# Optimization experiments

Hardware: AMD Instinct MI355X
Metric: run time of the kernel (lower is better)

## Reference

```python
import jax, jax.numpy as jnp
import numpy as np

# Model dims (from ModelArgs defaults)
B, S, DIM = 1, 1024, 2880
H, HKV, HD = 64, 8, 64        # query heads, kv heads, head dim
GROUP = H // HKV              # 8 query heads per kv head
WINDOW = 128                  # sliding window (layer_idx=0 -> active)
THETA = 150000.0


def setup_inputs() -> dict:
    key = jax.random.key(0)
    ks = jax.random.split(key, 10)
    rn = lambda k, shape, sc: (jax.random.normal(k, shape, jnp.float32) * sc)
    return {
        "x": rn(ks[0], (B, S, DIM), 1.0),
        "wq_w": rn(ks[1], (H * HD, DIM), 0.02),
        "wq_b": rn(ks[2], (H * HD,), 0.02),
        "wk_w": rn(ks[3], (HKV * HD, DIM), 0.02),
        "wk_b": rn(ks[4], (HKV * HD,), 0.02),
        "wv_w": rn(ks[5], (HKV * HD, DIM), 0.02),
        "wv_b": rn(ks[6], (HKV * HD,), 0.02),
        "wo_w": rn(ks[7], (DIM, H * HD), 0.02),
        "wo_b": rn(ks[8], (DIM,), 0.02),
        "sinks": rn(ks[9], (H,), 1.0),
    }


def _rope(t):
    # t: [B, S, h, HD]; half-split (rotate_half) RoPE with base THETA
    half = HD // 2
    inv_freq = 1.0 / (THETA ** (jnp.arange(half, dtype=jnp.float32) * 2.0 / HD))
    ang = jnp.arange(S, dtype=jnp.float32)[:, None] * inv_freq      # [S, half]
    cos = jnp.cos(ang)[None, :, None, :]
    sin = jnp.sin(ang)[None, :, None, :]
    t1, t2 = t[..., :half], t[..., half:]
    return jnp.concatenate([t1 * cos - t2 * sin, t1 * sin + t2 * cos], axis=-1)


def reference(x, wq_w, wq_b, wk_w, wk_b, wv_w, wv_b, wo_w, wo_b, sinks):
    # Projections (nn.Linear: y = x @ W^T + b)
    q = (jnp.einsum('bsd,ed->bse', x, wq_w) + wq_b).reshape(B, S, H, HD)
    k = (jnp.einsum('bsd,ed->bse', x, wk_w) + wk_b).reshape(B, S, HKV, HD)
    v = (jnp.einsum('bsd,ed->bse', x, wv_w) + wv_b).reshape(B, S, HKV, HD)

    q = _rope(q)
    k = _rope(k)

    # GQA: expand kv heads to match query heads
    k = jnp.repeat(k, GROUP, axis=2)   # [B, S, H, HD]
    v = jnp.repeat(v, GROUP, axis=2)

    scale = HD ** -0.5
    scores = jnp.einsum('bihd,bjhd->bhij', q, k) * scale   # [B, H, S, S]

    # Causal + sliding-window mask: attend to j with 0 <= i-j < WINDOW
    i = jnp.arange(S)[:, None]
    j = jnp.arange(S)[None, :]
    allowed = (j <= i) & ((i - j) < WINDOW)
    scores = jnp.where(allowed, scores, jnp.float32(-1e30))

    # Softmax with per-head learnable sink logit folded into normalization
    sink = sinks[None, :, None, None]                       # [1, H, 1, 1]
    m = jnp.maximum(jnp.max(scores, axis=-1, keepdims=True), sink)
    e = jnp.exp(scores - m)
    denom = jnp.sum(e, axis=-1, keepdims=True) + jnp.exp(sink - m)
    probs = e / denom                                       # sink mass dropped

    out = jnp.einsum('bhij,bjhd->bihd', probs, v).reshape(B, S, H * HD)
    return jnp.einsum('bse,de->bsd', out, wo_w) + wo_b
```

## Files before the change

### kernel.cpp

```cpp
#include <hip/hip_runtime.h>

typedef __attribute__((ext_vector_type(4))) float f32x4;
typedef __attribute__((ext_vector_type(8))) short s16x8;
typedef unsigned short u16;

#define DEVI __device__ __forceinline__

DEVI u16 f2bf(float f) {
    union { float f; unsigned int u; } v; v.f = f;
    unsigned int r = v.u + 0x7FFFu + ((v.u >> 16) & 1u);
    return (u16)(r >> 16);
}
DEVI float bf2f(u16 b) {
    union { unsigned int u; float f; } v; v.u = ((unsigned int)b) << 16;
    return v.f;
}

typedef __attribute__((address_space(1))) void gv_t;
typedef __attribute__((address_space(3))) void sv_t;

#define GLOAD16(SRC, DST) __builtin_amdgcn_global_load_lds( \
    (gv_t*)(SRC), (sv_t*)(DST), 16, 0, 0)

DEVI f32x4 mfma_bf16(s16x8 a, s16x8 b, f32x4 c) {
    return __builtin_amdgcn_mfma_f32_16x16x32_bf16(a, b, c, 0, 0, 0);
}

__global__ void cvt1_kernel(
    const float* __restrict__ x,  const float* __restrict__ wq, const float* __restrict__ wk,
    const float* __restrict__ wv,
    u16* __restrict__ xb, u16* __restrict__ wqb, u16* __restrict__ wkb,
    u16* __restrict__ wvb)
{
    int id = blockIdx.x * 256 + threadIdx.x;
    const float* s; u16* d; int off;
    if      (id < 737280)  { s = x;  d = xb;  off = id; }
    else if (id < 3686400) { s = wq; d = wqb; off = id - 737280; }
    else if (id < 4055040) { s = wk; d = wkb; off = id - 3686400; }
    else                   { s = wv; d = wvb; off = id - 4055040; }
    f32x4 v = *(const f32x4*)(s + (size_t)off * 4);
    union { u16 u[4]; unsigned long long ll; } o;
    #pragma unroll
    for (int j = 0; j < 4; ++j) o.u[j] = f2bf(v[j]);
    *(unsigned long long*)(d + (size_t)off * 4) = o.ll;
}

__global__ void cvt_wo_kernel(const float* __restrict__ wo, u16* __restrict__ wob)
{
    int id = blockIdx.x * 256 + threadIdx.x;
    f32x4 v = *(const f32x4*)(wo + (size_t)id * 4);
    union { u16 u[4]; unsigned long long ll; } o;
    #pragma unroll
    for (int j = 0; j < 4; ++j) o.u[j] = f2bf(v[j]);
    *(unsigned long long*)(wob + (size_t)id * 4) = o.ll;
}

__global__ __launch_bounds__(256, 2) void gemm_bf16nt(
    const u16* __restrict__ A, int lda, int kit, int ntot,
    const u16* __restrict__ W0, int t0, int n0, int c0,
    const u16* __restrict__ W1, int t1, int n1, int c1,
    const u16* __restrict__ W2, int t2, int n2, int c2,
    u16* __restrict__ C, int ldc, long long cstride)
{
    __shared__ u16 Als[2][128 * 64];
    __shared__ u16 Bls[2][128 * 64];

    const int lin = blockIdx.x;
    const int xc  = lin & 7;
    const int mm  = lin >> 3;
    const int nbl = xc + 8 * (mm >> 3);
    const int yt  = mm & 7;
    if (nbl >= ntot) return;

    const int tid  = threadIdx.x;
    const int lane = tid & 63;
    const int wid  = tid >> 6;
    const int li   = lane & 15;
    const int lg   = lane >> 4;
    const int m0   = yt * 128;

    const u16* W; int nt0, nsz, cb;
    if (nbl < t0)           { W = W0; nt0 = nbl * 128;             nsz = n0; cb = c0; }
    else if (nbl < t0 + t1) { W = W1; nt0 = (nbl - t0) * 128;      nsz = n1; cb = c1; }
    else                    { W = W2; nt0 = (nbl - t0 - t1) * 128; nsz = n2; cb = c2; }

    const int z  = blockIdx.z;
    const int S  = gridDim.z;
    const int it0 = (z * kit) / S;
    const int it1 = ((z + 1) * kit) / S;
    u16* Cp = C + (long long)z * cstride;

    const int wm = (wid >> 1) * 64;
    const int wn = (wid & 1) * 64;

    f32x4 acc[4][4];
    #pragma unroll
    for (int mi = 0; mi < 4; ++mi)
        #pragma unroll
        for (int ni = 0; ni < 4; ++ni)
            acc[mi][ni] = (f32x4){0.f, 0.f, 0.f, 0.f};

    const int srow = tid >> 3;
    const int slc  = (tid & 7) ^ (srow & 7);

#define STAGE(BUF, IT)                                                          \
    do {                                                                        \
        int k0_ = (IT) * 64;                                                    \
        _Pragma("unroll")                                                       \
        for (int s_ = 0; s_ < 4; ++s_) {                                        \
            const u16* sa_ = A + (size_t)(m0 + s_ * 32 + srow) * lda + k0_ + slc * 8; \
            GLOAD16(sa_, &Als[BUF][(s_ * 256 + wid * 64) * 8]);                 \
        }                                                                       \
        _Pragma("unroll")                                                       \
        for (int s_ = 0; s_ < 4; ++s_) {                                        \
            int wr_ = nt0 + s_ * 32 + srow;                                     \
            if (wr_ > nsz - 1) wr_ = nsz - 1;                                   \
            const u16* sb_ = W + (size_t)wr_ * lda + k0_ + slc * 8;             \
            GLOAD16(sb_, &Bls[BUF][(s_ * 256 + wid * 64) * 8]);                 \
        }                                                                       \
    } while (0)

    STAGE(0, it0);
    asm volatile("" ::: "memory");
    STAGE(1, it0 + 1);

    for (int it = it0; it < it1; ++it) {
        const int cur = (it - it0) & 1;

        if (it + 1 < it1) {
            asm volatile("s_waitcnt vmcnt(8)\n\ts_barrier" ::: "memory");
        } else {
            asm volatile("s_waitcnt vmcnt(0)\n\ts_barrier" ::: "memory");
        }

        s16x8 af[4][2], bfv[4][2];
        #pragma unroll
        for (int mi = 0; mi < 4; ++mi)
            #pragma unroll
            for (int kc = 0; kc < 2; ++kc) {
                int row = wm + mi * 16 + li;
                int ch  = (kc * 4 + lg) ^ (row & 7);
                af[mi][kc] = *(const s16x8*)&Als[cur][row * 64 + ch * 8];
            }
        #pragma unroll
        for (int ni = 0; ni < 4; ++ni)
            #pragma unroll
            for (int kc = 0; kc < 2; ++kc) {
                int row = wn + ni * 16 + li;
                int ch  = (kc * 4 + lg) ^ (row & 7);
                bfv[ni][kc] = *(const s16x8*)&Bls[cur][row * 64 + ch * 8];
            }
        #pragma unroll
        for (int mi = 0; mi < 4; ++mi)
            #pragma unroll
            for (int ni = 0; ni < 4; ++ni)
                #pragma unroll
                for (int kc = 0; kc < 2; ++kc)
                    acc[mi][ni] = mfma_bf16(af[mi][kc], bfv[ni][kc], acc[mi][ni]);

        asm volatile("s_waitcnt lgkmcnt(0)\n\ts_barrier" ::: "memory");

        if (it + 2 < it1) STAGE(cur, it + 2);
    }
#undef STAGE

    #pragma unroll
    for (int ni = 0; ni < 4; ++ni) {
        int colr = nt0 + wn + ni * 16 + li;
        if (colr < nsz) {
            #pragma unroll
            for (int mi = 0; mi < 4; ++mi)
                #pragma unroll
                for (int r = 0; r < 4; ++r) {
                    int row = m0 + wm + mi * 16 + lg * 4 + r;
                    Cp[(size_t)row * ldc + cb + colr] = f2bf(acc[mi][ni][r]);
                }
        }
    }
}

__global__ void rope_kernel(const u16* __restrict__ qkvp,
                            const float* __restrict__ qb, const float* __restrict__ kb,
                            const float* __restrict__ vb,
                            u16* __restrict__ qo, u16* __restrict__ ko, u16* __restrict__ vo)
{
    const long long PST = 1024LL * 5120;
    int id = blockIdx.x * 256 + threadIdx.x;
    int s  = id / 2560;
    int r  = id % 2560;
    const u16* r0 = qkvp + (size_t)s * 5120;
    if (r < 2304) {
        bool isq = r < 2048;
        int rr   = isq ? r : r - 2048;
        int hh   = rr >> 5;
        int d    = rr & 31;
        int col  = (isq ? 0 : 4096) + hh * 64 + d;
        int bcol = isq ? col : col - 4096;
        const float* bias = isq ? qb : kb;
        float t1 = bf2f(r0[col])      + bf2f(r0[col + PST])      + bf2f(r0[col + 2 * PST])      + bias[bcol];
        float t2 = bf2f(r0[col + 32]) + bf2f(r0[col + 32 + PST]) + bf2f(r0[col + 32 + 2 * PST]) + bias[bcol + 32];
        float ang = (float)s * exp2f((float)d * -0.5373314f);
        float sn, cs;
        sincosf(ang, &sn, &cs);
        float sc = isq ? 0.125f : 1.0f;
        float o1 = (t1 * cs - t2 * sn) * sc;
        float o2 = (t1 * sn + t2 * cs) * sc;
        u16* dst = isq ? qo : ko;
        int ldd  = isq ? 4096 : 512;
        dst[(size_t)s * ldd + bcol]      = f2bf(o1);
        dst[(size_t)s * ldd + bcol + 32] = f2bf(o2);
    } else {
        int e = (r - 2304) * 2;
        int c0 = 4608 + e;
        float v0 = bf2f(r0[c0])     + bf2f(r0[c0 + PST])     + bf2f(r0[c0 + 2 * PST])     + vb[e];
        float v1 = bf2f(r0[c0 + 1]) + bf2f(r0[c0 + 1 + PST]) + bf2f(r0[c0 + 1 + 2 * PST]) + vb[e + 1];
        vo[(size_t)s * 512 + e]     = f2bf(v0);
        vo[(size_t)s * 512 + e + 1] = f2bf(v1);
    }
}

__global__ void reduce_out_kernel(const u16* __restrict__ parts,
                                  const float* __restrict__ bias,
                                  float* __restrict__ out)
{
    int id = blockIdx.x * 256 + threadIdx.x;
    const long long stride = 1024LL * 2880;
    long long base = (long long)id * 8;
    float s[8];
    #pragma unroll
    for (int j = 0; j < 8; ++j) s[j] = 0.f;
    #pragma unroll
    for (int p = 0; p < 5; ++p) {
        s16x8 v = *(const s16x8*)(parts + p * stride + base);
        #pragma unroll
        for (int j = 0; j < 8; ++j) s[j] += bf2f((u16)v[j]);
    }
    int cb = (int)(base % 2880);
    f32x4 b0 = *(const f32x4*)(bias + cb);
    f32x4 b1 = *(const f32x4*)(bias + cb + 4);
    f32x4 o0 = {s[0] + b0[0], s[1] + b0[1], s[2] + b0[2], s[3] + b0[3]};
    f32x4 o1 = {s[4] + b1[0], s[5] + b1[1], s[6] + b1[2], s[7] + b1[3]};
    *(f32x4*)(out + base)     = o0;
    *(f32x4*)(out + base + 4) = o1;
}

__global__ __launch_bounds__(256, 2) void attn_kernel(
    const u16* __restrict__ Q, const u16* __restrict__ Kb, const u16* __restrict__ Vb,
    const float* __restrict__ sinks, u16* __restrict__ Ob)
{
    __shared__ u16 Kls[64 * 64];
    __shared__ u16 Pls[4][16 * 72];

    const int h    = blockIdx.x;
    const int qblk = blockIdx.y;
    const int kvh  = h >> 3;
    const int tid  = threadIdx.x;
    const int lane = tid & 63;
    const int w    = tid >> 6;
    const int li   = lane & 15;
    const int lg   = lane >> 4;
    const int qw   = qblk * 64 + w * 16;

    s16x8 aq[2];
    {
        const u16* qrow = Q + ((size_t)(qw + li) * 64 + h) * 64 + lg * 8;
        aq[0] = *(const s16x8*)(qrow);
        aq[1] = *(const s16x8*)(qrow + 32);
    }

    const float snk = sinks[h];
    float m_run[4], l_run[4];
    f32x4 oacc[4];
    #pragma unroll
    for (int r = 0; r < 4; ++r) { m_run[r] = snk; l_run[r] = 1.0f; }
    #pragma unroll
    for (int ni = 0; ni < 4; ++ni) oacc[ni] = (f32x4){0.f, 0.f, 0.f, 0.f};

    const int srow = tid >> 3;
    const int slc  = (tid & 7) ^ (srow & 7);

    for (int t = 0; t < 3; ++t) {
        int jt = qblk - 2 + t;
        if (jt < 0) continue;
        int j0 = jt * 64;

        #pragma unroll
        for (int it = 0; it < 2; ++it) {
            const u16* src = Kb + ((size_t)(j0 + it * 32 + srow) * 8 + kvh) * 64 + slc * 8;
            GLOAD16(src, &Kls[(it * 256 + w * 64) * 8]);
        }
        __syncthreads();

        f32x4 sc[4];
        #pragma unroll
        for (int nf = 0; nf < 4; ++nf) {
            sc[nf] = (f32x4){0.f, 0.f, 0.f, 0.f};
            #pragma unroll
            for (int kc = 0; kc < 2; ++kc) {
                int row = nf * 16 + li;
                int ch  = (kc * 4 + lg) ^ (row & 7);
                s16x8 bk = *(const s16x8*)&Kls[row * 64 + ch * 8];
                sc[nf] = mfma_bf16(aq[kc], bk, sc[nf]);
            }
        }

        #pragma unroll
        for (int r = 0; r < 4; ++r) {
            const int qg = qw + lg * 4 + r;
            float mx = -1e30f;
            #pragma unroll
            for (int nf = 0; nf < 4; ++nf) {
                int jg = j0 + nf * 16 + li;
                bool ok = (jg <= qg) && (qg - jg < 128);
                float v = ok ? sc[nf][r] : -1e30f;
                sc[nf][r] = v;
                mx = fmaxf(mx, v);
            }
            #pragma unroll
            for (int off = 1; off < 16; off <<= 1)
                mx = fmaxf(mx, __shfl_xor(mx, off));
            float mnew = fmaxf(m_run[r], mx);
            float corr = __expf(m_run[r] - mnew);
            m_run[r] = mnew;
            float rs = 0.f;
            #pragma unroll
            for (int nf = 0; nf < 4; ++nf) {
                float p = __expf(sc[nf][r] - mnew);
                rs += p;
                Pls[w][(lg * 4 + r) * 72 + nf * 16 + li] = f2bf(p);
            }
            #pragma unroll
            for (int off = 1; off < 16; off <<= 1)
                rs += __shfl_xor(rs, off);
            l_run[r] = l_run[r] * corr + rs;
            #pragma unroll
            for (int ni = 0; ni < 4; ++ni) oacc[ni][r] *= corr;
        }
        __syncthreads();

        #pragma unroll
        for (int kc = 0; kc < 2; ++kc) {
            s16x8 pa = *(const s16x8*)&Pls[w][li * 72 + kc * 32 + lg * 8];
            #pragma unroll
            for (int ni = 0; ni < 4; ++ni) {
                const u16* vsrc = Vb + ((size_t)(j0 + kc * 32 + lg * 8) * 8 + kvh) * 64 + ni * 16 + li;
                s16x8 bv;
                #pragma unroll
                for (int i = 0; i < 8; ++i) bv[i] = (short)vsrc[(size_t)i * 512];
                oacc[ni] = mfma_bf16(pa, bv, oacc[ni]);
            }
        }
    }

    #pragma unroll
    for (int r = 0; r < 4; ++r) {
        float inv = 1.0f / l_run[r];
        #pragma unroll
        for (int ni = 0; ni < 4; ++ni)
            Ob[((size_t)(qw + lg * 4 + r) * 64 + h) * 64 + ni * 16 + li] = f2bf(oacc[ni][r] * inv);
    }
}

extern "C" void kernel_launch(void* const* d_in, const int* in_sizes, int n_in,
                              void* d_out, int out_size, void* d_ws, size_t ws_size,
                              hipStream_t stream)
{
    const float* x     = (const float*)d_in[0];
    const float* wq_w  = (const float*)d_in[1];
    const float* wq_b  = (const float*)d_in[2];
    const float* wk_w  = (const float*)d_in[3];
    const float* wk_b  = (const float*)d_in[4];
    const float* wv_w  = (const float*)d_in[5];
    const float* wv_b  = (const float*)d_in[6];
    const float* wo_w  = (const float*)d_in[7];
    const float* wo_b  = (const float*)d_in[8];
    const float* sinks = (const float*)d_in[9];

    char* ws = (char*)d_ws;
    u16*   xb   = (u16*)(ws + 0);
    u16*   wqb  = (u16*)(ws + 5898240ULL);
    u16*   wkb  = (u16*)(ws + 29491200ULL);
    u16*   wvb  = (u16*)(ws + 32440320ULL);
    u16*   qkvp = (u16*)(ws + 35389440ULL);
    u16*   qr   = (u16*)(ws + 0);
    u16*   kr   = (u16*)(ws + 8388608ULL);
    u16*   vbf  = (u16*)(ws + 9437184ULL);
    u16*   attb = (u16*)(ws + 10485760ULL);
    u16*   wob  = (u16*)(ws + 35389440ULL);
    u16*   oprt = (u16*)(ws + 58982400ULL);

    (void)in_sizes; (void)n_in; (void)out_size; (void)ws_size;

    cvt1_kernel<<<17280, 256, 0, stream>>>(x, wq_w, wk_w, wv_w, xb, wqb, wkb, wvb);
    gemm_bf16nt<<<dim3(320, 1, 3), 256, 0, stream>>>(xb, 2880, 45, 40,
        wqb, 32, 4096, 0,
        wkb, 4, 512, 4096,
        wvb, 4, 512, 4608,
        qkvp, 5120, 1024LL * 5120);
    rope_kernel<<<10240, 256, 0, stream>>>(qkvp, wq_b, wk_b, wv_b, qr, kr, vbf);
    cvt_wo_kernel<<<11520, 256, 0, stream>>>(wo_w, wob);
    attn_kernel<<<dim3(64, 16), 256, 0, stream>>>(qr, kr, vbf, sinks, attb);
    gemm_bf16nt<<<dim3(192, 1, 5), 256, 0, stream>>>(attb, 4096, 64, 23,
        wob, 23, 2880, 0,
        wob, 0, 0, 0,
        wob, 0, 0, 0,
        oprt, 2880, 1024LL * 2880);
    reduce_out_kernel<<<1440, 256, 0, stream>>>(oprt, wo_b, (float*)d_out);
}
```

Measured before the change: 140.1 us.

## Use 8-wave GEMM blocks with smaller per-wave tiles; merge wo conversion into one kernel

The GEMM now runs 512 threads (8 waves) per 128x128 tile. Each wave computes a 64x32 sub-tile instead of 64x64, and staging issues two loads per operand per thread instead of four, with the vmcnt wait adjusted to match. This halves accumulator registers per wave and targets higher occupancy and better latency hiding, but each wave does less MFMA work per LDS read. The separate wo fp32-to-bf16 kernel is folded into the main conversion kernel, saving a launch. To allow this, wob moves to a new workspace offset so it no longer aliases qkvp.

```diff
diff --git a/kernel.cpp b/kernel.cpp
--- a/kernel.cpp
+++ b/kernel.cpp
@@ -26,18 +26,19 @@
     return __builtin_amdgcn_mfma_f32_16x16x32_bf16(a, b, c, 0, 0, 0);
 }
 
-__global__ void cvt1_kernel(
+__global__ void cvt_all_kernel(
     const float* __restrict__ x,  const float* __restrict__ wq, const float* __restrict__ wk,
-    const float* __restrict__ wv,
+    const float* __restrict__ wv, const float* __restrict__ wo,
     u16* __restrict__ xb, u16* __restrict__ wqb, u16* __restrict__ wkb,
-    u16* __restrict__ wvb)
+    u16* __restrict__ wvb, u16* __restrict__ wob)
 {
     int id = blockIdx.x * 256 + threadIdx.x;
     const float* s; u16* d; int off;
     if      (id < 737280)  { s = x;  d = xb;  off = id; }
     else if (id < 3686400) { s = wq; d = wqb; off = id - 737280; }
     else if (id < 4055040) { s = wk; d = wkb; off = id - 3686400; }
-    else                   { s = wv; d = wvb; off = id - 4055040; }
+    else if (id < 4423680) { s = wv; d = wvb; off = id - 4055040; }
+    else                   { s = wo; d = wob; off = id - 4423680; }
     f32x4 v = *(const f32x4*)(s + (size_t)off * 4);
     union { u16 u[4]; unsigned long long ll; } o;
     #pragma unroll
@@ -45,17 +46,7 @@
     *(unsigned long long*)(d + (size_t)off * 4) = o.ll;
 }
 
-__global__ void cvt_wo_kernel(const float* __restrict__ wo, u16* __restrict__ wob)
-{
-    int id = blockIdx.x * 256 + threadIdx.x;
-    f32x4 v = *(const f32x4*)(wo + (size_t)id * 4);
-    union { u16 u[4]; unsigned long long ll; } o;
-    #pragma unroll
-    for (int j = 0; j < 4; ++j) o.u[j] = f2bf(v[j]);
-    *(unsigned long long*)(wob + (size_t)id * 4) = o.ll;
-}
-
-__global__ __launch_bounds__(256, 2) void gemm_bf16nt(
+__global__ __launch_bounds__(512, 4) void gemm_bf16nt(
     const u16* __restrict__ A, int lda, int kit, int ntot,
     const u16* __restrict__ W0, int t0, int n0, int c0,
     const u16* __restrict__ W1, int t1, int n1, int c1,
@@ -90,33 +81,36 @@
     const int it1 = ((z + 1) * kit) / S;
     u16* Cp = C + (long long)z * cstride;
 
-    const int wm = (wid >> 1) * 64;
-    const int wn = (wid & 1) * 64;
-
-    f32x4 acc[4][4];
+    const int wm = (wid >> 2) * 64;
+    const int wn = (wid & 3) * 32;
+
+    f32x4 acc[4][2];
     #pragma unroll
     for (int mi = 0; mi < 4; ++mi)
         #pragma unroll
-        for (int ni = 0; ni < 4; ++ni)
+        for (int ni = 0; ni < 2; ++ni)
             acc[mi][ni] = (f32x4){0.f, 0.f, 0.f, 0.f};
-
-    const int srow = tid >> 3;
-    const int slc  = (tid & 7) ^ (srow & 7);
 
 #define STAGE(BUF, IT)                                                          \
     do {                                                                        \
         int k0_ = (IT) * 64;                                                    \
         _Pragma("unroll")                                                       \
-        for (int s_ = 0; s_ < 4; ++s_) {                                        \
-            const u16* sa_ = A + (size_t)(m0 + s_ * 32 + srow) * lda + k0_ + slc * 8; \
-            GLOAD16(sa_, &Als[BUF][(s_ * 256 + wid * 64) * 8]);                 \
+        for (int s_ = 0; s_ < 2; ++s_) {                                        \
+            int g_   = s_ * 512 + tid;                                          \
+            int row_ = g_ >> 3;                                                 \
+            int cs_  = (tid & 7) ^ (row_ & 7);                                  \
+            const u16* sa_ = A + (size_t)(m0 + row_) * lda + k0_ + cs_ * 8;     \
+            GLOAD16(sa_, &Als[BUF][g_ * 8]);                                    \
         }                                                                       \
         _Pragma("unroll")                                                       \
-        for (int s_ = 0; s_ < 4; ++s_) {                                        \
-            int wr_ = nt0 + s_ * 32 + srow;                                     \
-            if (wr_ > nsz - 1) wr_ = nsz - 1;                                   \
-            const u16* sb_ = W + (size_t)wr_ * lda + k0_ + slc * 8;             \
-            GLOAD16(sb_, &Bls[BUF][(s_ * 256 + wid * 64) * 8]);                 \
+        for (int s_ = 0; s_ < 2; ++s_) {                                        \
+            int g_   = s_ * 512 + tid;                                          \
+            int row_ = g_ >> 3;                                                 \
+            int wr_  = nt0 + row_;                                              \
+            if (wr_ > nsz - 1) wr_ = nsz - 1;               \
+            int cs_  = (tid & 7) ^ (row_ & 7);                                  \
+            const u16* sb_ = W + (size_t)wr_ * lda + k0_ + cs_ * 8;             \
+            GLOAD16(sb_, &Bls[BUF][g_ * 8]);                                    \
         }                                                                       \
     } while (0)
 
@@ -128,12 +122,12 @@
         const int cur = (it - it0) & 1;
 
         if (it + 1 < it1) {
-            asm volatile("s_waitcnt vmcnt(8)\n\ts_barrier" ::: "memory");
+            asm volatile("s_waitcnt vmcnt(4)\n\ts_barrier" ::: "memory");
         } else {
             asm volatile("s_waitcnt vmcnt(0)\n\ts_barrier" ::: "memory");
         }
 
-        s16x8 af[4][2], bfv[4][2];
+        s16x8 af[4][2], bfv[2][2];
         #pragma unroll
         for (int mi = 0; mi < 4; ++mi)
             #pragma unroll
@@ -143,7 +137,7 @@
                 af[mi][kc] = *(const s16x8*)&Als[cur][row * 64 + ch * 8];
             }
         #pragma unroll
-        for (int ni = 0; ni < 4; ++ni)
+        for (int ni = 0; ni < 2; ++ni)
             #pragma unroll
             for (int kc = 0; kc < 2; ++kc) {
                 int row = wn + ni * 16 + li;
@@ -153,7 +147,7 @@
         #pragma unroll
         for (int mi = 0; mi < 4; ++mi)
             #pragma unroll
-            for (int ni = 0; ni < 4; ++ni)
+            for (int ni = 0; ni < 2; ++ni)
                 #pragma unroll
                 for (int kc = 0; kc < 2; ++kc)
                     acc[mi][ni] = mfma_bf16(af[mi][kc], bfv[ni][kc], acc[mi][ni]);
@@ -165,7 +159,7 @@
 #undef STAGE
 
     #pragma unroll
-    for (int ni = 0; ni < 4; ++ni) {
+    for (int ni = 0; ni < 2; ++ni) {
         int colr = nt0 + wn + ni * 16 + li;
         if (colr < nsz) {
             #pragma unroll
@@ -386,21 +380,21 @@
     u16*   kr   = (u16*)(ws + 8388608ULL);
     u16*   vbf  = (u16*)(ws + 9437184ULL);
     u16*   attb = (u16*)(ws + 10485760ULL);
-    u16*   wob  = (u16*)(ws + 35389440ULL);
     u16*   oprt = (u16*)(ws + 58982400ULL);
+    u16*   wob  = (u16*)(ws + 88473600ULL);
 
     (void)in_sizes; (void)n_in; (void)out_size; (void)ws_size;
 
-    cvt1_kernel<<<17280, 256, 0, stream>>>(x, wq_w, wk_w, wv_w, xb, wqb, wkb, wvb);
-    gemm_bf16nt<<<dim3(320, 1, 3), 256, 0, stream>>>(xb, 2880, 45, 40,
+    cvt_all_kernel<<<28800, 256, 0, stream>>>(x, wq_w, wk_w, wv_w, wo_w,
+                                              xb, wqb, wkb, wvb, wob);
+    gemm_bf16nt<<<dim3(320, 1, 3), 512, 0, stream>>>(xb, 2880, 45, 40,
         wqb, 32, 4096, 0,
         wkb, 4, 512, 4096,
         wvb, 4, 512, 4608,
         qkvp, 5120, 1024LL * 5120);
     rope_kernel<<<10240, 256, 0, stream>>>(qkvp, wq_b, wk_b, wv_b, qr, kr, vbf);
-    cvt_wo_kernel<<<11520, 256, 0, stream>>>(wo_w, wob);
     attn_kernel<<<dim3(64, 16), 256, 0, stream>>>(qr, kr, vbf, sinks, attb);
-    gemm_bf16nt<<<dim3(192, 1, 5), 256, 0, stream>>>(attb, 4096, 64, 23,
+    gemm_bf16nt<<<dim3(192, 1, 5), 512, 0, stream>>>(attb, 4096, 64, 23,
         wob, 23, 2880, 0,
         wob, 0, 0, 0,
         wob, 0, 0, 0,
```

Result: no change. 138.8 us (-1.0%).
